# Optimization experiments

Measured on AMD Instinct MI355X. Metric: run time of the kernel, lower is better.

## Reference

```python
import jax, jax.numpy as jnp
import numpy as np
import math

NUM_HEADS = 16
HIDDEN = 1024
HEAD_DIM = HIDDEN // NUM_HEADS
WIN = 512  # relative position window size
B, S = 2, 2048
LN_EPS = 1e-5


def setup_inputs() -> dict:
    key = jax.random.key(0)
    ks = jax.random.split(key, 8)
    sd = 1.0 / math.sqrt(HIDDEN)
    return {
        "x": jax.random.normal(ks[0], (B, S, HIDDEN), jnp.float32),
        "Wq": jax.random.normal(ks[1], (HIDDEN, HIDDEN), jnp.float32) * sd,
        "bq": jnp.zeros((HIDDEN,), jnp.float32),
        "Wk": jax.random.normal(ks[2], (HIDDEN, HIDDEN), jnp.float32) * sd,
        "bk": jnp.zeros((HIDDEN,), jnp.float32),
        "Wv": jax.random.normal(ks[3], (HIDDEN, HIDDEN), jnp.float32) * sd,
        "bv": jnp.zeros((HIDDEN,), jnp.float32),
        "Wo": jax.random.normal(ks[4], (HIDDEN, HIDDEN), jnp.float32) * sd,
        "bo": jnp.zeros((HIDDEN,), jnp.float32),
        "relpos_table": jax.random.normal(ks[5], (WIN, HIDDEN), jnp.float32),
        "ln_gamma": jnp.ones((HIDDEN,), jnp.float32),
        "ln_beta": jnp.zeros((HIDDEN,), jnp.float32),
        "Wrk": jax.random.normal(ks[6], (HIDDEN, HIDDEN), jnp.float32) * sd,
        "brk": jnp.zeros((HIDDEN,), jnp.float32),
        "Wrq": jax.random.normal(ks[7], (HIDDEN, HIDDEN), jnp.float32) * sd,
        "brq": jnp.zeros((HIDDEN,), jnp.float32),
    }


def reference(x, Wq, bq, Wk, bk, Wv, bv, Wo, bo,
              relpos_table, ln_gamma, ln_beta, Wrk, brk, Wrq, brq):
    Bsz, Slen, H = x.shape
    nh, hd = NUM_HEADS, HEAD_DIM

    # QKV projections -> [B, S, nh, hd]
    q = (x @ Wq + bq).reshape(Bsz, Slen, nh, hd)
    k = (x @ Wk + bk).reshape(Bsz, Slen, nh, hd)
    v = (x @ Wv + bv).reshape(Bsz, Slen, nh, hd)

    mu = relpos_table.mean(-1, keepdims=True)
    var = relpos_table.var(-1, keepdims=True)  # biased, as in torch LayerNorm
    e = (relpos_table - mu) * jax.lax.rsqrt(var + LN_EPS) * ln_gamma + ln_beta

    # relative position index matrix [S, S]: clamp(key - query, -W+1, 0) + W-1
    qi = jnp.arange(Slen)
    relpos = jnp.clip(qi[None, :] - qi[:, None], -WIN + 1, 0) + (WIN - 1)

    rk = (e @ Wrk + brk).reshape(WIN, nh, hd)
    rq = (e @ Wrq + brq).reshape(WIN, nh, hd)

    # content-to-content scores [B, nh, S, S]
    c2c = jnp.einsum('bqhd,bkhd->bhqk', q, k)

    # content-to-position: scores over window then gather along window axis
    qps = jnp.einsum('bnhd,whd->bhnw', q, rk)           # [B, nh, S, W]
    c2p = qps[:, :, qi[:, None], relpos]                # [B, nh, S, S]

    # position-to-content: window x key_seq scores, gather along window axis
    kps = jnp.einsum('bnhd,whd->bhwn', k, rq)           # [B, nh, W, S]
    p2c = kps[:, :, relpos, qi[None, :]]                # [B, nh, S, S]

    scale_factor = 3.0  # 1 + relpos_q_enabled + relpos_k_enabled
    logits = (c2c + c2p + p2c) / math.sqrt(hd * scale_factor)

    # causal mask
    causal = qi[None, :] <= qi[:, None]
    logits = jnp.where(causal[None, None], logits, jnp.finfo(logits.dtype).min)

    attn = jax.nn.softmax(logits, axis=-1)              # [B, nh, S, S]
    out = jnp.einsum('bhqk,bkhd->bqhd', attn, v).reshape(Bsz, Slen, H)
    return out @ Wo + bo
```

## Files before the change

kernel.cpp:

```cpp
#include <hip/hip_runtime.h>
#include <math.h>

#define NH 16
#define HD 64
#define HID 1024
#define SEQ 2048
#define NB 2

typedef __attribute__((ext_vector_type(8))) short short8;
typedef __attribute__((ext_vector_type(4))) float f32x4;
typedef unsigned short u16;
typedef unsigned int u32;

constexpr float LN_EPS_C = 1e-5f;
constexpr float SM_SCALE = 0.07216878364870323f;

__device__ inline u16 f2b(float f) {
  unsigned u = __builtin_bit_cast(unsigned, f);
  u = (u + 0x7FFFu + ((u >> 16) & 1u)) >> 16;
  return (u16)u;
}
__device__ inline float b2f(u16 h) {
  unsigned u = ((unsigned)h) << 16;
  return __builtin_bit_cast(float, u);
}
__device__ inline u32 pk2(float lo, float hi) {
  return (u32)f2b(lo) | ((u32)f2b(hi) << 16);
}
__device__ inline f32x4 mfma16(short8 a, short8 b, f32x4 c) {
  return __builtin_amdgcn_mfma_f32_16x16x32_bf16(a, b, c, 0, 0, 0);
}
__device__ inline short8 swz8(const u16* base, int row, int hc) {
  return *reinterpret_cast<const short8*>(&base[row * 64 + 8 * (hc ^ (row & 7))]);
}
__device__ inline int vrot(int row, int col) {
  return row * 72 + ((col + 16 * ((row >> 3) & 3)) & 63);
}
template <int N>
__device__ inline float rorf(float x) {
  return __builtin_bit_cast(float,
      __builtin_amdgcn_update_dpp(0, __builtin_bit_cast(int, x),
                                  0x120 + N, 0xF, 0xF, true));
}
__device__ inline float rmax16(float x) {
  x = fmaxf(x, rorf<1>(x)); x = fmaxf(x, rorf<2>(x));
  x = fmaxf(x, rorf<4>(x)); x = fmaxf(x, rorf<8>(x));
  return x;
}
__device__ inline float rsum16(float x) {
  x += rorf<1>(x); x += rorf<2>(x); x += rorf<4>(x); x += rorf<8>(x);
  return x;
}

__global__ __launch_bounds__(256) void ln_kernel(const float* __restrict__ tbl,
    const float* __restrict__ gamma, const float* __restrict__ beta,
    u16* __restrict__ e) {
  int row = blockIdx.x;
  int t = threadIdx.x;
  const float4* rp = reinterpret_cast<const float4*>(tbl + (size_t)row * HID);
  float4 x = rp[t];
  float s = x.x + x.y + x.z + x.w;
  float ss = x.x * x.x + x.y * x.y + x.z * x.z + x.w * x.w;
  #pragma unroll
  for (int o = 1; o < 64; o <<= 1) {
    s += __shfl_xor(s, o);
    ss += __shfl_xor(ss, o);
  }
  __shared__ float sb[4], ssb[4];
  int w = t >> 6;
  if ((t & 63) == 0) { sb[w] = s; ssb[w] = ss; }
  __syncthreads();
  s = sb[0] + sb[1] + sb[2] + sb[3];
  ss = ssb[0] + ssb[1] + ssb[2] + ssb[3];
  float mu = s * (1.0f / HID);
  float var = ss * (1.0f / HID) - mu * mu;
  float rs = rsqrtf(var + LN_EPS_C);
  float4 g = reinterpret_cast<const float4*>(gamma)[t];
  float4 bt = reinterpret_cast<const float4*>(beta)[t];
  ushort4 o4;
  o4.x = f2b((x.x - mu) * rs * g.x + bt.x);
  o4.y = f2b((x.y - mu) * rs * g.y + bt.y);
  o4.z = f2b((x.z - mu) * rs * g.z + bt.z);
  o4.w = f2b((x.w - mu) * rs * g.w + bt.w);
  *reinterpret_cast<ushort4*>(&e[(size_t)row * HID + t * 4]) = o4;
}

__global__ __launch_bounds__(256) void conv_bf16(const float* __restrict__ src,
    u16* __restrict__ dst, int n) {
  int i = (blockIdx.x * 256 + threadIdx.x) * 8;
  if (i >= n) return;
  float4 a = *reinterpret_cast<const float4*>(&src[i]);
  float4 c = *reinterpret_cast<const float4*>(&src[i + 4]);
  short8 o;
  o[0] = (short)f2b(a.x); o[1] = (short)f2b(a.y); o[2] = (short)f2b(a.z); o[3] = (short)f2b(a.w);
  o[4] = (short)f2b(c.x); o[5] = (short)f2b(c.y); o[6] = (short)f2b(c.z); o[7] = (short)f2b(c.w);
  *reinterpret_cast<short8*>(&dst[i]) = o;
}

struct P6 {
  const float* s[6];
  u16* d[6];
};
__global__ __launch_bounds__(256) void transp_all(P6 p) {
  __shared__ float T[32][33];
  const float* W = p.s[blockIdx.z];
  u16* Wt = p.d[blockIdx.z];
  int bn = blockIdx.x * 32, bk = blockIdx.y * 32;
  int t = threadIdx.x;
  int r = t >> 3, c4 = (t & 7) * 4;
  float4 v = *reinterpret_cast<const float4*>(&W[(size_t)(bk + r) * HID + bn + c4]);
  T[r][c4 + 0] = v.x; T[r][c4 + 1] = v.y; T[r][c4 + 2] = v.z; T[r][c4 + 3] = v.w;
  __syncthreads();
  int n = t >> 3, k4 = (t & 7) * 4;
  ushort4 o;
  o.x = f2b(T[k4 + 0][n]); o.y = f2b(T[k4 + 1][n]);
  o.z = f2b(T[k4 + 2][n]); o.w = f2b(T[k4 + 3][n]);
  *reinterpret_cast<ushort4*>(&Wt[(size_t)(bn + n) * HID + bk + k4]) = o;
}

struct GO {
  const float* bias[3];
  void* out[3];
};
template <bool F32OUT>
__global__ __launch_bounds__(512) void gemm_bf16(const u16* __restrict__ A,
    const u16* __restrict__ Bt, GO go) {
  __shared__ u16 Al[8192];
  __shared__ u16 Bl[8192];
  int t = threadIdx.x;
  int gx = gridDim.x;
  int nwg = gx * gridDim.y;
  int lin = blockIdx.y * gx + blockIdx.x;
  lin = (lin & 7) * (nwg >> 3) + (lin >> 3);
  int cb = (lin % gx) * 128, rb = (lin / gx) * 128;
  int which = cb >> 10, cbl = cb & 1023;
  const float* bias = go.bias[which];
  void* Cout = go.out[which];
  int wv = t >> 6, lane = t & 63, l15 = lane & 15, lg = lane >> 4;
  int wr = (wv >> 2) * 64, wc = (wv & 3) * 32;
  int srow = t >> 2, sch = t & 3;
  f32x4 acc[4][2];
  #pragma unroll
  for (int i = 0; i < 4; ++i)
    #pragma unroll
    for (int j = 0; j < 2; ++j) acc[i][j] = (f32x4){0.f, 0.f, 0.f, 0.f};
  const u16* Ap = A + (size_t)(rb + srow) * HID;
  const u16* Bp = Bt + (size_t)(cb + srow) * HID;
  int slot0 = 8 * (sch ^ (srow & 7));
  int slot1 = 8 * ((sch + 4) ^ (srow & 7));
  short8 pa0 = *reinterpret_cast<const short8*>(&Ap[sch * 8]);
  short8 pa1 = *reinterpret_cast<const short8*>(&Ap[(sch + 4) * 8]);
  short8 pb0 = *reinterpret_cast<const short8*>(&Bp[sch * 8]);
  short8 pb1 = *reinterpret_cast<const short8*>(&Bp[(sch + 4) * 8]);
  for (int kk = 0; kk < HID; kk += 64) {
    __syncthreads();
    *reinterpret_cast<short8*>(&Al[srow * 64 + slot0]) = pa0;
    *reinterpret_cast<short8*>(&Al[srow * 64 + slot1]) = pa1;
    *reinterpret_cast<short8*>(&Bl[srow * 64 + slot0]) = pb0;
    *reinterpret_cast<short8*>(&Bl[srow * 64 + slot1]) = pb1;
    __syncthreads();
    if (kk + 64 < HID) {
      pa0 = *reinterpret_cast<const short8*>(&Ap[kk + 64 + sch * 8]);
      pa1 = *reinterpret_cast<const short8*>(&Ap[kk + 64 + (sch + 4) * 8]);
      pb0 = *reinterpret_cast<const short8*>(&Bp[kk + 64 + sch * 8]);
      pb1 = *reinterpret_cast<const short8*>(&Bp[kk + 64 + (sch + 4) * 8]);
    }
    #pragma unroll
    for (int s = 0; s < 2; ++s) {
      short8 am[4], bn[2];
      #pragma unroll
      for (int i = 0; i < 4; ++i) am[i] = swz8(Al, wr + i * 16 + l15, s * 4 + lg);
      #pragma unroll
      for (int j = 0; j < 2; ++j) bn[j] = swz8(Bl, wc + j * 16 + l15, s * 4 + lg);
      #pragma unroll
      for (int i = 0; i < 4; ++i)
        #pragma unroll
        for (int j = 0; j < 2; ++j)
          acc[i][j] = mfma16(am[i], bn[j], acc[i][j]);
    }
  }
  #pragma unroll
  for (int j = 0; j < 2; ++j) {
    float bv = bias[cbl + wc + j * 16 + l15];
    #pragma unroll
    for (int i = 0; i < 4; ++i) {
      #pragma unroll
      for (int r = 0; r < 4; ++r) {
        size_t idx = (size_t)(rb + wr + i * 16 + lg * 4 + r) * HID + cbl + wc + j * 16 + l15;
        float v = acc[i][j][r] + bv;
        if (F32OUT) reinterpret_cast<float*>(Cout)[idx] = v;
        else reinterpret_cast<u16*>(Cout)[idx] = f2b(v);
      }
    }
  }
}

template <bool F32OUT>
__global__ __launch_bounds__(256) void gemm_m64(const u16* __restrict__ A,
    const u16* __restrict__ Bt, GO go) {
  __shared__ u16 Al[4096];
  __shared__ u16 Bl[8192];
  int t = threadIdx.x;
  int gx = gridDim.x;
  int nwg = gx * gridDim.y;
  int lin = blockIdx.y * gx + blockIdx.x;
  lin = (lin & 7) * (nwg >> 3) + (lin >> 3);
  int cb = (lin % gx) * 128, rb = (lin / gx) * 64;
  int which = cb >> 10, cbl = cb & 1023;
  const float* bias = go.bias[which];
  void* Cout = go.out[which];
  int wv = t >> 6, lane = t & 63, l15 = lane & 15, lg = lane >> 4;
  int wc = wv * 32;
  int arow = t >> 2, ach = t & 3;
  int aslot0 = 8 * (ach ^ (arow & 7));
  int aslot1 = 8 * ((ach + 4) ^ (arow & 7));
  int brow = t >> 1, bch = (t & 1) * 4;
  const u16* Ap = A + (size_t)(rb + arow) * HID;
  const u16* Bp = Bt + (size_t)(cb + brow) * HID;
  f32x4 acc[4][2];
  #pragma unroll
  for (int i = 0; i < 4; ++i)
    #pragma unroll
    for (int j = 0; j < 2; ++j) acc[i][j] = (f32x4){0.f, 0.f, 0.f, 0.f};
  short8 pa0 = *reinterpret_cast<const short8*>(&Ap[ach * 8]);
  short8 pa1 = *reinterpret_cast<const short8*>(&Ap[(ach + 4) * 8]);
  short8 pb[4];
  #pragma unroll
  for (int j = 0; j < 4; ++j)
    pb[j] = *reinterpret_cast<const short8*>(&Bp[(bch + j) * 8]);
  for (int kk = 0; kk < HID; kk += 64) {
    __syncthreads();
    *reinterpret_cast<short8*>(&Al[arow * 64 + aslot0]) = pa0;
    *reinterpret_cast<short8*>(&Al[arow * 64 + aslot1]) = pa1;
    #pragma unroll
    for (int j = 0; j < 4; ++j)
      *reinterpret_cast<short8*>(&Bl[brow * 64 + 8 * ((bch + j) ^ (brow & 7))]) = pb[j];
    __syncthreads();
    if (kk + 64 < HID) {
      pa0 = *reinterpret_cast<const short8*>(&Ap[kk + 64 + ach * 8]);
      pa1 = *reinterpret_cast<const short8*>(&Ap[kk + 64 + (ach + 4) * 8]);
      #pragma unroll
      for (int j = 0; j < 4; ++j)
        pb[j] = *reinterpret_cast<const short8*>(&Bp[kk + 64 + (bch + j) * 8]);
    }
    #pragma unroll
    for (int s = 0; s < 2; ++s) {
      short8 am[4], bn[2];
      #pragma unroll
      for (int i = 0; i < 4; ++i) am[i] = swz8(Al, i * 16 + l15, s * 4 + lg);
      #pragma unroll
      for (int j = 0; j < 2; ++j) bn[j] = swz8(Bl, wc + j * 16 + l15, s * 4 + lg);
      #pragma unroll
      for (int i = 0; i < 4; ++i)
        #pragma unroll
        for (int j = 0; j < 2; ++j)
          acc[i][j] = mfma16(am[i], bn[j], acc[i][j]);
    }
  }
  #pragma unroll
  for (int j = 0; j < 2; ++j) {
    float bv = bias[cbl + wc + j * 16 + l15];
    #pragma unroll
    for (int i = 0; i < 4; ++i) {
      #pragma unroll
      for (int r = 0; r < 4; ++r) {
        size_t idx = (size_t)(rb + i * 16 + lg * 4 + r) * HID + cbl + wc + j * 16 + l15;
        float v = acc[i][j][r] + bv;
        if (F32OUT) reinterpret_cast<float*>(Cout)[idx] = v;
        else reinterpret_cast<u16*>(Cout)[idx] = f2b(v);
      }
    }
  }
}

__global__ __launch_bounds__(256) void biasqk(const u16* __restrict__ Qb,
    const u16* __restrict__ Kb, const u16* __restrict__ RKb,
    const u16* __restrict__ RQb, float* __restrict__ qrk0,
    float* __restrict__ krq0) {
  int o = blockIdx.x * 64 + (threadIdx.x >> 2);
  int sub = threadIdx.x & 3;
  int b = o >> 15, h = (o >> 11) & 15, i = o & 2047;
  size_t rbase = (size_t)(b * SEQ + i) * HID + h * HD + sub * 16;
  size_t tbase = (size_t)h * HD + sub * 16;
  float s1 = 0.f, s2 = 0.f;
  #pragma unroll
  for (int c = 0; c < 2; ++c) {
    short8 qv = *reinterpret_cast<const short8*>(&Qb[rbase + c * 8]);
    short8 rv = *reinterpret_cast<const short8*>(&RKb[tbase + c * 8]);
    short8 kv = *reinterpret_cast<const short8*>(&Kb[rbase + c * 8]);
    short8 uv = *reinterpret_cast<const short8*>(&RQb[tbase + c * 8]);
    #pragma unroll
    for (int j = 0; j < 8; ++j) {
      s1 += b2f((u16)qv[j]) * b2f((u16)rv[j]);
      s2 += b2f((u16)kv[j]) * b2f((u16)uv[j]);
    }
  }
  s1 += __shfl_xor(s1, 1); s1 += __shfl_xor(s1, 2);
  s2 += __shfl_xor(s2, 1); s2 += __shfl_xor(s2, 2);
  if (sub == 0) { qrk0[o] = s1 * SM_SCALE; krq0[o] = s2 * SM_SCALE; }
}

__global__ __launch_bounds__(256, 3) void bias_kernel(
    const u16* __restrict__ Qb, const u16* __restrict__ Kb,
    const u16* __restrict__ RKb, const u16* __restrict__ RQb,
    u16* __restrict__ bandT) {
  __shared__ u16 smem[20992];
  const int KsO = 0, UO = 4096;
  const int RKO = UO, RQO = UO + 8192;
  const int G1O = UO, G2O = UO + 8448;

  int qt = blockIdx.x;
  int h = blockIdx.y, b = blockIdx.z;
  int q0 = qt * 64;
  int t = threadIdx.x;
  int wv = t >> 6, lane = t & 63, l15 = lane & 15, lg = lane >> 4;
  int qs = q0 + wv * 16;
  int hoff = h * HD;

  size_t qgrow = (size_t)(b * SEQ + qs + l15) * HID + hoff;
  short8 aq0 = *reinterpret_cast<const short8*>(&Qb[qgrow + lg * 8]);
  short8 aq1 = *reinterpret_cast<const short8*>(&Qb[qgrow + 32 + lg * 8]);

  const f32x4 Z = (f32x4){0.f, 0.f, 0.f, 0.f};
  int vr = t >> 2, vc8 = (t & 3) * 8;
  int ktlo = qt - 8; if (ktlo < 0) ktlo = 0;
  size_t tbase = (((size_t)(b * NH + h) * 32 + qt) * 9) << 12;

  for (int kt = ktlo; kt <= qt; ++kt) {
    int k0 = kt * 64;
    int dt = qt - kt;
    int wlo = 448 - 64 * dt; if (wlo < 0) wlo = 0;
    __syncthreads();
    {
      const u16* kg = &Kb[(size_t)(b * SEQ + k0 + vr) * HID + hoff];
      int c0 = vc8 >> 3;
      *reinterpret_cast<short8*>(&smem[KsO + vr * 64 + 8 * (c0 ^ (vr & 7))]) =
          *reinterpret_cast<const short8*>(&kg[vc8]);
      *reinterpret_cast<short8*>(&smem[KsO + vr * 64 + 8 * ((c0 + 4) ^ (vr & 7))]) =
          *reinterpret_cast<const short8*>(&kg[vc8 + 32]);
    }
    for (int e2 = t; e2 < 1024; e2 += 256) {
      int rr = e2 >> 3, cch = e2 & 7;
      int wr2 = wlo + rr; if (wr2 > 511) wr2 = 511;
      size_t gb = (size_t)wr2 * HID + hoff + cch * 8;
      int slot = 8 * (cch ^ (rr & 7));
      *reinterpret_cast<short8*>(&smem[RKO + rr * 64 + slot]) =
          *reinterpret_cast<const short8*>(&RKb[gb]);
      *reinterpret_cast<short8*>(&smem[RQO + rr * 64 + slot]) =
          *reinterpret_cast<const short8*>(&RQb[gb]);
    }
    __syncthreads();
    u32 g1p[16], g2p[16];
    #pragma unroll
    for (int cw = 0; cw < 8; ++cw) {
      short8 r0 = swz8(&smem[RKO], cw * 16 + l15, lg);
      short8 r1 = swz8(&smem[RKO], cw * 16 + l15, 4 + lg);
      f32x4 g = mfma16(r1, aq1, mfma16(r0, aq0, Z));
      g1p[2 * cw] = pk2(g[0], g[1]);
      g1p[2 * cw + 1] = pk2(g[2], g[3]);
    }
    short8 kw0 = swz8(&smem[KsO], wv * 16 + l15, lg);
    short8 kw1 = swz8(&smem[KsO], wv * 16 + l15, 4 + lg);
    #pragma unroll
    for (int cw = 0; cw < 8; ++cw) {
      short8 u0 = swz8(&smem[RQO], cw * 16 + l15, lg);
      short8 u1 = swz8(&smem[RQO], cw * 16 + l15, 4 + lg);
      f32x4 g = mfma16(u1, kw1, mfma16(u0, kw0, Z));
      g2p[2 * cw] = pk2(g[0], g[1]);
      g2p[2 * cw + 1] = pk2(g[2], g[3]);
    }
    __syncthreads();
    #pragma unroll
    for (int cw = 0; cw < 8; ++cw) {
      *reinterpret_cast<uint2*>(&smem[G1O + (wv * 16 + l15) * 132 + cw * 16 + lg * 4]) =
          make_uint2(g1p[2 * cw], g1p[2 * cw + 1]);
      *reinterpret_cast<uint2*>(&smem[G2O + (wv * 16 + l15) * 132 + cw * 16 + lg * 4]) =
          make_uint2(g2p[2 * cw], g2p[2 * cw + 1]);
    }
    __syncthreads();
    u16* outp = bandT + tbase + ((size_t)dt << 12) + t * 16;
    #pragma unroll
    for (int c = 0; c < 4; ++c) {
      float vv[4];
      #pragma unroll
      for (int r = 0; r < 4; ++r) {
        int q = qs + lg * 4 + r;
        int k = k0 + c * 16 + l15;
        int wi = 511 - (q - k) - wlo; if (wi < 0) wi = 0;
        vv[r] = (b2f(smem[G1O + (wv * 16 + lg * 4 + r) * 132 + wi]) +
                 b2f(smem[G2O + (c * 16 + l15) * 132 + wi])) * SM_SCALE;
      }
      *reinterpret_cast<uint2*>(outp + c * 4) =
          make_uint2(pk2(vv[0], vv[1]), pk2(vv[2], vv[3]));
    }
  }
}

__global__ __launch_bounds__(256, 2) void attn_mfma(
    const u16* __restrict__ Qb, const u16* __restrict__ Kb,
    const u16* __restrict__ Vb, const float* __restrict__ qrk0,
    const float* __restrict__ krq0, const u16* __restrict__ bandT,
    u16* __restrict__ ATT) {
  __shared__ u16 smem[22016];
  const int KsB[2] = {0, 4096};
  const int VtB[2] = {8192, 12800};
  const int PsO = 17408;

  int qtA = 31 - (int)blockIdx.x;
  int qtB = (int)blockIdx.x;
  int h = blockIdx.y, b = blockIdx.z;
  int t = threadIdx.x;
  int wv = t >> 6, lane = t & 63, l15 = lane & 15, lg = lane >> 4;
  int hoff = h * HD;
  int bh = (b * NH + h) * SEQ;
  size_t tbaseA = (((size_t)(b * NH + h) * 32 + qtA) * 9) << 12;
  size_t tbaseB = (((size_t)(b * NH + h) * 32 + qtB) * 9) << 12;

  int qsA = qtA * 64 + wv * 16;
  int qsB = qtB * 64 + wv * 16;
  size_t qgA = (size_t)(b * SEQ + qsA + l15) * HID + hoff;
  size_t qgB = (size_t)(b * SEQ + qsB + l15) * HID + hoff;
  short8 aqA0 = *reinterpret_cast<const short8*>(&Qb[qgA + lg * 8]);
  short8 aqA1 = *reinterpret_cast<const short8*>(&Qb[qgA + 32 + lg * 8]);
  short8 aqB0 = *reinterpret_cast<const short8*>(&Qb[qgB + lg * 8]);
  short8 aqB1 = *reinterpret_cast<const short8*>(&Qb[qgB + 32 + lg * 8]);
  float qb0A[4], qb0B[4];
  #pragma unroll
  for (int r = 0; r < 4; ++r) {
    qb0A[r] = qrk0[bh + qsA + lg * 4 + r];
    qb0B[r] = qrk0[bh + qsB + lg * 4 + r];
  }

  float mA[4], lA[4], mB[4], lB[4];
  f32x4 oA[4], oB[4];
  #pragma unroll
  for (int r = 0; r < 4; ++r) { mA[r] = -INFINITY; lA[r] = 0.f; mB[r] = -INFINITY; lB[r] = 0.f; }
  #pragma unroll
  for (int c = 0; c < 4; ++c) {
    oA[c] = (f32x4){0.f, 0.f, 0.f, 0.f};
    oB[c] = (f32x4){0.f, 0.f, 0.f, 0.f};
  }

  const f32x4 Z = (f32x4){0.f, 0.f, 0.f, 0.f};
  int vr = t >> 2, vc8 = (t & 3) * 8;
  int c0s = vc8 >> 3;
  int kslot0 = vr * 64 + 8 * (c0s ^ (vr & 7));
  int kslot1 = vr * 64 + 8 * ((c0s + 4) ^ (vr & 7));
  int vslot[16];
  #pragma unroll
  for (int j = 0; j < 8; ++j) {
    vslot[j] = vrot(vc8 + j, vr);
    vslot[8 + j] = vrot(vc8 + 32 + j, vr);
  }

  {
    const u16* kg = &Kb[(size_t)(b * SEQ + vr) * HID + hoff];
    short8 k0v = *reinterpret_cast<const short8*>(&kg[vc8]);
    short8 k1v = *reinterpret_cast<const short8*>(&kg[vc8 + 32]);
    *reinterpret_cast<short8*>(&smem[KsB[0] + kslot0]) = k0v;
    *reinterpret_cast<short8*>(&smem[KsB[0] + kslot1]) = k1v;
    const u16* vg = &Vb[(size_t)(b * SEQ + vr) * HID + hoff];
    short8 v0v = *reinterpret_cast<const short8*>(&vg[vc8]);
    short8 v1v = *reinterpret_cast<const short8*>(&vg[vc8 + 32]);
    #pragma unroll
    for (int j = 0; j < 8; ++j) smem[VtB[0] + vslot[j]] = (u16)v0v[j];
    #pragma unroll
    for (int j = 0; j < 8; ++j) smem[VtB[0] + vslot[8 + j]] = (u16)v1v[j];
  }
  __syncthreads();

  int cur = 0;
  for (int kt = 0; kt <= qtA; ++kt) {
    int k0 = kt * 64;
    int dtA = qtA - kt;
    bool doB = (kt <= qtB);
    int dtB = qtB - kt;
    bool bandedA = (dtA <= 8);
    bool bandedB = doB && (dtB <= 8);
    int ksb = KsB[cur], vtb = VtB[cur];
    int ksn = KsB[cur ^ 1], vtn = VtB[cur ^ 1];

    short8 pA0, pA1, pB0, pB1;
    if (bandedA) {
      const u16* tb = bandT + tbaseA + ((size_t)dtA << 12) + t * 16;
      pA0 = *reinterpret_cast<const short8*>(tb);
      pA1 = *reinterpret_cast<const short8*>(tb + 8);
    }
    if (bandedB) {
      const u16* tb = bandT + tbaseB + ((size_t)dtB << 12) + t * 16;
      pB0 = *reinterpret_cast<const short8*>(tb);
      pB1 = *reinterpret_cast<const short8*>(tb + 8);
    }
    float kq[4];
    if (dtA > 8 || (doB && dtB > 8)) {
      #pragma unroll
      for (int c = 0; c < 4; ++c) kq[c] = krq0[bh + k0 + c * 16 + l15];
    }
    short8 nk0, nk1, nv0, nv1;
    if (kt < qtA) {
      const u16* kg = &Kb[(size_t)(b * SEQ + k0 + 64 + vr) * HID + hoff];
      nk0 = *reinterpret_cast<const short8*>(&kg[vc8]);
      nk1 = *reinterpret_cast<const short8*>(&kg[vc8 + 32]);
      const u16* vg = &Vb[(size_t)(b * SEQ + k0 + 64 + vr) * HID + hoff];
      nv0 = *reinterpret_cast<const short8*>(&vg[vc8]);
      nv1 = *reinterpret_cast<const short8*>(&vg[vc8 + 32]);
    }

    short8 kb0[4], kb1[4];
    #pragma unroll
    for (int c = 0; c < 4; ++c) {
      kb0[c] = swz8(&smem[ksb], c * 16 + l15, lg);
      kb1[c] = swz8(&smem[ksb], c * 16 + l15, 4 + lg);
    }
    f32x4 sA[4], sB[4];
    #pragma unroll
    for (int c = 0; c < 4; ++c)
      sA[c] = mfma16(aqA1, kb1[c], mfma16(aqA0, kb0[c], Z));
    if (doB) {
      #pragma unroll
      for (int c = 0; c < 4; ++c)
        sB[c] = mfma16(aqB1, kb1[c], mfma16(aqB0, kb0[c], Z));
    }
    #pragma unroll
    for (int c = 0; c < 4; ++c) {
      #pragma unroll
      for (int r = 0; r < 4; ++r) {
        float bbv = bandedA ? b2f((u16)((c < 2 ? pA0 : pA1)[(c & 1) * 4 + r]))
                            : qb0A[r] + kq[c];
        float v = fmaf(sA[c][r], SM_SCALE, bbv);
        if (dtA == 0) {
          int ql = wv * 16 + lg * 4 + r, kl = c * 16 + l15;
          if (ql < kl) v = -INFINITY;
        }
        sA[c][r] = v;
      }
    }
    if (doB) {
      #pragma unroll
      for (int c = 0; c < 4; ++c) {
        #pragma unroll
        for (int r = 0; r < 4; ++r) {
          float bbv = bandedB ? b2f((u16)((c < 2 ? pB0 : pB1)[(c & 1) * 4 + r]))
                              : qb0B[r] + kq[c];
          float v = fmaf(sB[c][r], SM_SCALE, bbv);
          if (dtB == 0) {
            int ql = wv * 16 + lg * 4 + r, kl = c * 16 + l15;
            if (ql < kl) v = -INFINITY;
          }
          sB[c][r] = v;
        }
      }
    }
    float alA[4], alB[4];
    #pragma unroll
    for (int r = 0; r < 4; ++r) {
      float mx = fmaxf(fmaxf(sA[0][r], sA[1][r]), fmaxf(sA[2][r], sA[3][r]));
      mx = rmax16(mx);
      float mn = fmaxf(mA[r], mx);
      alA[r] = __expf(mA[r] - mn);
      float ps = 0.f;
      #pragma unroll
      for (int c = 0; c < 4; ++c) {
        float p = __expf(sA[c][r] - mn);
        sA[c][r] = p;
        ps += p;
      }
      ps = rsum16(ps);
      lA[r] = lA[r] * alA[r] + ps;
      mA[r] = mn;
    }
    if (doB) {
      #pragma unroll
      for (int r = 0; r < 4; ++r) {
        float mx = fmaxf(fmaxf(sB[0][r], sB[1][r]), fmaxf(sB[2][r], sB[3][r]));
        mx = rmax16(mx);
        float mn = fmaxf(mB[r], mx);
        alB[r] = __expf(mB[r] - mn);
        float ps = 0.f;
        #pragma unroll
        for (int c = 0; c < 4; ++c) {
          float p = __expf(sB[c][r] - mn);
          sB[c][r] = p;
          ps += p;
        }
        ps = rsum16(ps);
        lB[r] = lB[r] * alB[r] + ps;
        mB[r] = mn;
      }
    }
    short8 vb0[4], vb1[4];
    #pragma unroll
    for (int c = 0; c < 4; ++c) {
      int n = c * 16 + l15;
      vb0[c] = *reinterpret_cast<const short8*>(&smem[vtb + vrot(n, lg * 8)]);
      vb1[c] = *reinterpret_cast<const short8*>(&smem[vtb + vrot(n, 32 + lg * 8)]);
    }
    #pragma unroll
    for (int c = 0; c < 4; ++c) {
      #pragma unroll
      for (int r = 0; r < 4; ++r) {
        smem[PsO + vrot(wv * 16 + lg * 4 + r, c * 16 + l15)] = f2b(sA[c][r]);
        oA[c][r] *= alA[r];
      }
    }
    int prow = wv * 16 + l15;
    {
      short8 ap0 = *reinterpret_cast<const short8*>(&smem[PsO + vrot(prow, lg * 8)]);
      short8 ap1 = *reinterpret_cast<const short8*>(&smem[PsO + vrot(prow, 32 + lg * 8)]);
      #pragma unroll
      for (int c = 0; c < 4; ++c)
        oA[c] = mfma16(ap1, vb1[c], mfma16(ap0, vb0[c], oA[c]));
    }
    if (doB) {
      #pragma unroll
      for (int c = 0; c < 4; ++c) {
        #pragma unroll
        for (int r = 0; r < 4; ++r) {
          smem[PsO + vrot(wv * 16 + lg * 4 + r, c * 16 + l15)] = f2b(sB[c][r]);
          oB[c][r] *= alB[r];
        }
      }
      short8 bp0 = *reinterpret_cast<const short8*>(&smem[PsO + vrot(prow, lg * 8)]);
      short8 bp1 = *reinterpret_cast<const short8*>(&smem[PsO + vrot(prow, 32 + lg * 8)]);
      #pragma unroll
      for (int c = 0; c < 4; ++c)
        oB[c] = mfma16(bp1, vb1[c], mfma16(bp0, vb0[c], oB[c]));
    }
    if (kt < qtA) {
      *reinterpret_cast<short8*>(&smem[ksn + kslot0]) = nk0;
      *reinterpret_cast<short8*>(&smem[ksn + kslot1]) = nk1;
      #pragma unroll
      for (int j = 0; j < 8; ++j) smem[vtn + vslot[j]] = (u16)nv0[j];
      #pragma unroll
      for (int j = 0; j < 8; ++j) smem[vtn + vslot[8 + j]] = (u16)nv1[j];
    }
    __syncthreads();
    cur ^= 1;
  }
  #pragma unroll
  for (int r = 0; r < 4; ++r) { lA[r] = 1.0f / lA[r]; lB[r] = 1.0f / lB[r]; }
  #pragma unroll
  for (int c = 0; c < 4; ++c) {
    #pragma unroll
    for (int r = 0; r < 4; ++r) {
      size_t obA = (size_t)(b * SEQ + qsA + lg * 4 + r) * HID + hoff + c * 16 + l15;
      ATT[obA] = f2b(oA[c][r] * lA[r]);
      size_t obB = (size_t)(b * SEQ + qsB + lg * 4 + r) * HID + hoff + c * 16 + l15;
      ATT[obB] = f2b(oB[c][r] * lB[r]);
    }
  }
}

extern "C" void kernel_launch(void* const* d_in, const int* in_sizes, int n_in,
                              void* d_out, int out_size, void* d_ws, size_t ws_size,
                              hipStream_t stream) {
  const float* x      = (const float*)d_in[0];
  const float* Wq     = (const float*)d_in[1];
  const float* bq     = (const float*)d_in[2];
  const float* Wk     = (const float*)d_in[3];
  const float* bk     = (const float*)d_in[4];
  const float* Wv     = (const float*)d_in[5];
  const float* bv     = (const float*)d_in[6];
  const float* Wo     = (const float*)d_in[7];
  const float* bo     = (const float*)d_in[8];
  const float* relpos = (const float*)d_in[9];
  const float* gamma  = (const float*)d_in[10];
  const float* beta   = (const float*)d_in[11];
  const float* Wrk    = (const float*)d_in[12];
  const float* brk    = (const float*)d_in[13];
  const float* Wrq    = (const float*)d_in[14];
  const float* brq    = (const float*)d_in[15];
  float* out = (float*)d_out;

  u16* wsu = (u16*)d_ws;
  size_t off = 0;
  auto alloc = [&](size_t n) { u16* p = wsu + off; off += n; return p; };
  u16* xb   = alloc(4194304);
  u16* Eb   = alloc(524288);
  u16* WtQ  = alloc(1048576);
  u16* WtK  = alloc(1048576);
  u16* WtV  = alloc(1048576);
  u16* WtO  = alloc(1048576);
  u16* WtRK = alloc(1048576);
  u16* WtRQ = alloc(1048576);
  u16* Qb2  = alloc(4194304);
  u16* Kb2  = alloc(4194304);
  u16* Vb2  = alloc(4194304);
  u16* ATTb = alloc(4194304);
  u16* RKb2 = alloc(524288);
  u16* RQb2 = alloc(524288);
  float* qrk0 = (float*)(wsu + off); off += 131072;
  float* krq0 = (float*)(wsu + off); off += 131072;
  u16* bandT = alloc((size_t)NB * NH * 32 * 9 * 4096);

  ln_kernel<<<512, 256, 0, stream>>>(relpos, gamma, beta, Eb);
  conv_bf16<<<2048, 256, 0, stream>>>(x, xb, 4194304);
  P6 p6;
  p6.s[0] = Wq; p6.s[1] = Wk; p6.s[2] = Wv; p6.s[3] = Wo; p6.s[4] = Wrk; p6.s[5] = Wrq;
  p6.d[0] = WtQ; p6.d[1] = WtK; p6.d[2] = WtV; p6.d[3] = WtO; p6.d[4] = WtRK; p6.d[5] = WtRQ;
  dim3 gT(32, 32, 6);
  transp_all<<<gT, 256, 0, stream>>>(p6);

  GO goQKV = {{bq, bk, bv}, {Qb2, Kb2, Vb2}};
  dim3 gQKV(24, 32);
  gemm_bf16<false><<<gQKV, 512, 0, stream>>>(xb, WtQ, goQKV);
  GO goRel = {{brk, brq, brq}, {RKb2, RQb2, RQb2}};
  dim3 gRel2(16, 8);
  gemm_m64<false><<<gRel2, 256, 0, stream>>>(Eb, WtRK, goRel);

  biasqk<<<1024, 256, 0, stream>>>(Qb2, Kb2, RKb2, RQb2, qrk0, krq0);

  dim3 gB(32, NH, NB);
  bias_kernel<<<gB, 256, 0, stream>>>(Qb2, Kb2, RKb2, RQb2, bandT);

  dim3 gA(16, NH, NB);
  attn_mfma<<<gA, 256, 0, stream>>>(Qb2, Kb2, Vb2, qrk0, krq0, bandT, ATTb);

  GO goOut = {{bo, bo, bo}, {out, out, out}};
  dim3 gOut(8, 64);
  gemm_m64<true><<<gOut, 256, 0, stream>>>(ATTb, WtO, goOut);
}
```

Before: 219.9 us.

## Merge prep kernels, fold biasqk into bias kernel, skip unchanged softmax rescale

Combines the layernorm, input conversion and weight transpose launches into one prep kernel that dispatches on block index. Computes the per-row qrk0/krq0 bias scalars inside bias_kernel instead of a separate launch. In the attention loop, the online-softmax rescale of the accumulators is skipped when no row max changes across the wavefront. Together these remove three launches and some multiplies, at the cost of a branch and a wave vote per tile.

```diff
diff --git a/kernel.cpp b/kernel.cpp
--- a/kernel.cpp
+++ b/kernel.cpp
@@ -52,70 +52,67 @@
   return x;
 }
 
-__global__ __launch_bounds__(256) void ln_kernel(const float* __restrict__ tbl,
-    const float* __restrict__ gamma, const float* __restrict__ beta,
-    u16* __restrict__ e) {
-  int row = blockIdx.x;
+struct PrepArgs {
+  const float* tbl; const float* gamma; const float* beta; u16* e;
+  const float* x; u16* xb;
+  const float* ws[6]; u16* wd[6];
+};
+__global__ __launch_bounds__(256) void prep_kernel(PrepArgs p) {
+  __shared__ float T[32][33];
+  __shared__ float sb[4], ssb[4];
+  int bid = blockIdx.x;
   int t = threadIdx.x;
-  const float4* rp = reinterpret_cast<const float4*>(tbl + (size_t)row * HID);
-  float4 x = rp[t];
-  float s = x.x + x.y + x.z + x.w;
-  float ss = x.x * x.x + x.y * x.y + x.z * x.z + x.w * x.w;
-  #pragma unroll
-  for (int o = 1; o < 64; o <<= 1) {
-    s += __shfl_xor(s, o);
-    ss += __shfl_xor(ss, o);
-  }
-  __shared__ float sb[4], ssb[4];
-  int w = t >> 6;
-  if ((t & 63) == 0) { sb[w] = s; ssb[w] = ss; }
-  __syncthreads();
-  s = sb[0] + sb[1] + sb[2] + sb[3];
-  ss = ssb[0] + ssb[1] + ssb[2] + ssb[3];
-  float mu = s * (1.0f / HID);
-  float var = ss * (1.0f / HID) - mu * mu;
-  float rs = rsqrtf(var + LN_EPS_C);
-  float4 g = reinterpret_cast<const float4*>(gamma)[t];
-  float4 bt = reinterpret_cast<const float4*>(beta)[t];
-  ushort4 o4;
-  o4.x = f2b((x.x - mu) * rs * g.x + bt.x);
-  o4.y = f2b((x.y - mu) * rs * g.y + bt.y);
-  o4.z = f2b((x.z - mu) * rs * g.z + bt.z);
-  o4.w = f2b((x.w - mu) * rs * g.w + bt.w);
-  *reinterpret_cast<ushort4*>(&e[(size_t)row * HID + t * 4]) = o4;
-}
-
-__global__ __launch_bounds__(256) void conv_bf16(const float* __restrict__ src,
-    u16* __restrict__ dst, int n) {
-  int i = (blockIdx.x * 256 + threadIdx.x) * 8;
-  if (i >= n) return;
-  float4 a = *reinterpret_cast<const float4*>(&src[i]);
-  float4 c = *reinterpret_cast<const float4*>(&src[i + 4]);
-  short8 o;
-  o[0] = (short)f2b(a.x); o[1] = (short)f2b(a.y); o[2] = (short)f2b(a.z); o[3] = (short)f2b(a.w);
-  o[4] = (short)f2b(c.x); o[5] = (short)f2b(c.y); o[6] = (short)f2b(c.z); o[7] = (short)f2b(c.w);
-  *reinterpret_cast<short8*>(&dst[i]) = o;
-}
-
-struct P6 {
-  const float* s[6];
-  u16* d[6];
-};
-__global__ __launch_bounds__(256) void transp_all(P6 p) {
-  __shared__ float T[32][33];
-  const float* W = p.s[blockIdx.z];
-  u16* Wt = p.d[blockIdx.z];
-  int bn = blockIdx.x * 32, bk = blockIdx.y * 32;
-  int t = threadIdx.x;
-  int r = t >> 3, c4 = (t & 7) * 4;
-  float4 v = *reinterpret_cast<const float4*>(&W[(size_t)(bk + r) * HID + bn + c4]);
-  T[r][c4 + 0] = v.x; T[r][c4 + 1] = v.y; T[r][c4 + 2] = v.z; T[r][c4 + 3] = v.w;
-  __syncthreads();
-  int n = t >> 3, k4 = (t & 7) * 4;
-  ushort4 o;
-  o.x = f2b(T[k4 + 0][n]); o.y = f2b(T[k4 + 1][n]);
-  o.z = f2b(T[k4 + 2][n]); o.w = f2b(T[k4 + 3][n]);
-  *reinterpret_cast<ushort4*>(&Wt[(size_t)(bn + n) * HID + bk + k4]) = o;
+  if (bid < 512) {
+    int row = bid;
+    const float4* rp = reinterpret_cast<const float4*>(p.tbl + (size_t)row * HID);
+    float4 x = rp[t];
+    float s = x.x + x.y + x.z + x.w;
+    float ss = x.x * x.x + x.y * x.y + x.z * x.z + x.w * x.w;
+    #pragma unroll
+    for (int o = 1; o < 64; o <<= 1) {
+      s += __shfl_xor(s, o);
+      ss += __shfl_xor(ss, o);
+    }
+    int w = t >> 6;
+    if ((t & 63) == 0) { sb[w] = s; ssb[w] = ss; }
+    __syncthreads();
+    s = sb[0] + sb[1] + sb[2] + sb[3];
+    ss = ssb[0] + ssb[1] + ssb[2] + ssb[3];
+    float mu = s * (1.0f / HID);
+    float var = ss * (1.0f / HID) - mu * mu;
+    float rs = rsqrtf(var + LN_EPS_C);
+    float4 g = reinterpret_cast<const float4*>(p.gamma)[t];
+    float4 bt = reinterpret_cast<const float4*>(p.beta)[t];
+    ushort4 o4;
+    o4.x = f2b((x.x - mu) * rs * g.x + bt.x);
+    o4.y = f2b((x.y - mu) * rs * g.y + bt.y);
+    o4.z = f2b((x.z - mu) * rs * g.z + bt.z);
+    o4.w = f2b((x.w - mu) * rs * g.w + bt.w);
+    *reinterpret_cast<ushort4*>(&p.e[(size_t)row * HID + t * 4]) = o4;
+  } else if (bid < 2560) {
+    int i = ((bid - 512) * 256 + t) * 8;
+    float4 a = *reinterpret_cast<const float4*>(&p.x[i]);
+    float4 c = *reinterpret_cast<const float4*>(&p.x[i + 4]);
+    short8 o;
+    o[0] = (short)f2b(a.x); o[1] = (short)f2b(a.y); o[2] = (short)f2b(a.z); o[3] = (short)f2b(a.w);
+    o[4] = (short)f2b(c.x); o[5] = (short)f2b(c.y); o[6] = (short)f2b(c.z); o[7] = (short)f2b(c.w);
+    *reinterpret_cast<short8*>(&p.xb[i]) = o;
+  } else {
+    int z = (bid - 2560) >> 10;
+    int rem = (bid - 2560) & 1023;
+    int bn = (rem & 31) * 32, bk = (rem >> 5) * 32;
+    const float* W = p.ws[z];
+    u16* Wt = p.wd[z];
+    int r = t >> 3, c4 = (t & 7) * 4;
+    float4 v = *reinterpret_cast<const float4*>(&W[(size_t)(bk + r) * HID + bn + c4]);
+    T[r][c4 + 0] = v.x; T[r][c4 + 1] = v.y; T[r][c4 + 2] = v.z; T[r][c4 + 3] = v.w;
+    __syncthreads();
+    int n = t >> 3, k4 = (t & 7) * 4;
+    ushort4 o;
+    o.x = f2b(T[k4 + 0][n]); o.y = f2b(T[k4 + 1][n]);
+    o.z = f2b(T[k4 + 2][n]); o.w = f2b(T[k4 + 3][n]);
+    *reinterpret_cast<ushort4*>(&Wt[(size_t)(bn + n) * HID + bk + k4]) = o;
+  }
 }
 
 struct GO {
@@ -273,37 +270,11 @@
   }
 }
 
-__global__ __launch_bounds__(256) void biasqk(const u16* __restrict__ Qb,
-    const u16* __restrict__ Kb, const u16* __restrict__ RKb,
-    const u16* __restrict__ RQb, float* __restrict__ qrk0,
-    float* __restrict__ krq0) {
-  int o = blockIdx.x * 64 + (threadIdx.x >> 2);
-  int sub = threadIdx.x & 3;
-  int b = o >> 15, h = (o >> 11) & 15, i = o & 2047;
-  size_t rbase = (size_t)(b * SEQ + i) * HID + h * HD + sub * 16;
-  size_t tbase = (size_t)h * HD + sub * 16;
-  float s1 = 0.f, s2 = 0.f;
-  #pragma unroll
-  for (int c = 0; c < 2; ++c) {
-    short8 qv = *reinterpret_cast<const short8*>(&Qb[rbase + c * 8]);
-    short8 rv = *reinterpret_cast<const short8*>(&RKb[tbase + c * 8]);
-    short8 kv = *reinterpret_cast<const short8*>(&Kb[rbase + c * 8]);
-    short8 uv = *reinterpret_cast<const short8*>(&RQb[tbase + c * 8]);
-    #pragma unroll
-    for (int j = 0; j < 8; ++j) {
-      s1 += b2f((u16)qv[j]) * b2f((u16)rv[j]);
-      s2 += b2f((u16)kv[j]) * b2f((u16)uv[j]);
-    }
-  }
-  s1 += __shfl_xor(s1, 1); s1 += __shfl_xor(s1, 2);
-  s2 += __shfl_xor(s2, 1); s2 += __shfl_xor(s2, 2);
-  if (sub == 0) { qrk0[o] = s1 * SM_SCALE; krq0[o] = s2 * SM_SCALE; }
-}
-
 __global__ __launch_bounds__(256, 3) void bias_kernel(
     const u16* __restrict__ Qb, const u16* __restrict__ Kb,
     const u16* __restrict__ RKb, const u16* __restrict__ RQb,
-    u16* __restrict__ bandT) {
+    u16* __restrict__ bandT, float* __restrict__ qrk0,
+    float* __restrict__ krq0) {
   __shared__ u16 smem[20992];
   const int KsO = 0, UO = 4096;
   const int RKO = UO, RQO = UO + 8192;
@@ -316,6 +287,30 @@
   int wv = t >> 6, lane = t & 63, l15 = lane & 15, lg = lane >> 4;
   int qs = q0 + wv * 16;
   int hoff = h * HD;
+  int bh = (b * NH + h) * SEQ;
+
+  {
+    int i = q0 + (t >> 2);
+    int sub = t & 3;
+    size_t rbase = (size_t)(b * SEQ + i) * HID + hoff + sub * 16;
+    size_t tb2 = (size_t)hoff + sub * 16;
+    float s1 = 0.f, s2 = 0.f;
+    #pragma unroll
+    for (int c = 0; c < 2; ++c) {
+      short8 qv = *reinterpret_cast<const short8*>(&Qb[rbase + c * 8]);
+      short8 rv = *reinterpret_cast<const short8*>(&RKb[tb2 + c * 8]);
+      short8 kv = *reinterpret_cast<const short8*>(&Kb[rbase + c * 8]);
+      short8 uv = *reinterpret_cast<const short8*>(&RQb[tb2 + c * 8]);
+      #pragma unroll
+      for (int j = 0; j < 8; ++j) {
+        s1 += b2f((u16)qv[j]) * b2f((u16)rv[j]);
+        s2 += b2f((u16)kv[j]) * b2f((u16)uv[j]);
+      }
+    }
+    s1 += __shfl_xor(s1, 1); s1 += __shfl_xor(s1, 2);
+    s2 += __shfl_xor(s2, 1); s2 += __shfl_xor(s2, 2);
+    if (sub == 0) { qrk0[bh + i] = s1 * SM_SCALE; krq0[bh + i] = s2 * SM_SCALE; }
+  }
 
   size_t qgrow = (size_t)(b * SEQ + qs + l15) * HID + hoff;
   short8 aq0 = *reinterpret_cast<const short8*>(&Qb[qgrow + lg * 8]);
@@ -551,41 +546,70 @@
         }
       }
     }
-    float alA[4], alB[4];
-    #pragma unroll
-    for (int r = 0; r < 4; ++r) {
-      float mx = fmaxf(fmaxf(sA[0][r], sA[1][r]), fmaxf(sA[2][r], sA[3][r]));
-      mx = rmax16(mx);
-      float mn = fmaxf(mA[r], mx);
-      alA[r] = __expf(mA[r] - mn);
-      float ps = 0.f;
-      #pragma unroll
-      for (int c = 0; c < 4; ++c) {
-        float p = __expf(sA[c][r] - mn);
-        sA[c][r] = p;
-        ps += p;
-      }
-      ps = rsum16(ps);
-      lA[r] = lA[r] * alA[r] + ps;
-      mA[r] = mn;
+    {
+      float mn[4];
+      #pragma unroll
+      for (int r = 0; r < 4; ++r) {
+        float mx = fmaxf(fmaxf(sA[0][r], sA[1][r]), fmaxf(sA[2][r], sA[3][r]));
+        mx = rmax16(mx);
+        mn[r] = fmaxf(mA[r], mx);
+      }
+      bool sk = (mn[0] == mA[0]) && (mn[1] == mA[1]) &&
+                (mn[2] == mA[2]) && (mn[3] == mA[3]);
+      if (!__all(sk)) {
+        #pragma unroll
+        for (int r = 0; r < 4; ++r) {
+          float al = __expf(mA[r] - mn[r]);
+          lA[r] *= al;
+          mA[r] = mn[r];
+          #pragma unroll
+          for (int c = 0; c < 4; ++c) oA[c][r] *= al;
+        }
+      }
+      #pragma unroll
+      for (int r = 0; r < 4; ++r) {
+        float ps = 0.f;
+        #pragma unroll
+        for (int c = 0; c < 4; ++c) {
+          float p = __expf(sA[c][r] - mA[r]);
+          sA[c][r] = p;
+          ps += p;
+        }
+        ps = rsum16(ps);
+        lA[r] += ps;
+      }
     }
     if (doB) {
+      float mn[4];
       #pragma unroll
       for (int r = 0; r < 4; ++r) {
         float mx = fmaxf(fmaxf(sB[0][r], sB[1][r]), fmaxf(sB[2][r], sB[3][r]));
         mx = rmax16(mx);
-        float mn = fmaxf(mB[r], mx);
-        alB[r] = __expf(mB[r] - mn);
+        mn[r] = fmaxf(mB[r], mx);
+      }
+      bool sk = (mn[0] == mB[0]) && (mn[1] == mB[1]) &&
+                (mn[2] == mB[2]) && (mn[3] == mB[3]);
+      if (!__all(sk)) {
+        #pragma unroll
+        for (int r = 0; r < 4; ++r) {
+          float al = __expf(mB[r] - mn[r]);
+          lB[r] *= al;
+          mB[r] = mn[r];
+          #pragma unroll
+          for (int c = 0; c < 4; ++c) oB[c][r] *= al;
+        }
+      }
+      #pragma unroll
+      for (int r = 0; r < 4; ++r) {
         float ps = 0.f;
         #pragma unroll
         for (int c = 0; c < 4; ++c) {
-          float p = __expf(sB[c][r] - mn);
+          float p = __expf(sB[c][r] - mB[r]);
           sB[c][r] = p;
           ps += p;
         }
         ps = rsum16(ps);
-        lB[r] = lB[r] * alB[r] + ps;
-        mB[r] = mn;
+        lB[r] += ps;
       }
     }
     short8 vb0[4], vb1[4];
@@ -596,13 +620,10 @@
       vb1[c] = *reinterpret_cast<const short8*>(&smem[vtb + vrot(n, 32 + lg * 8)]);
     }
     #pragma unroll
-    for (int c = 0; c < 4; ++c) {
-      #pragma unroll
-      for (int r = 0; r < 4; ++r) {
+    for (int c = 0; c < 4; ++c)
+      #pragma unroll
+      for (int r = 0; r < 4; ++r)
         smem[PsO + vrot(wv * 16 + lg * 4 + r, c * 16 + l15)] = f2b(sA[c][r]);
-        oA[c][r] *= alA[r];
-      }
-    }
     int prow = wv * 16 + l15;
     {
       short8 ap0 = *reinterpret_cast<const short8*>(&smem[PsO + vrot(prow, lg * 8)]);
@@ -613,13 +634,10 @@
     }
     if (doB) {
       #pragma unroll
-      for (int c = 0; c < 4; ++c) {
+      for (int c = 0; c < 4; ++c)
         #pragma unroll
-        for (int r = 0; r < 4; ++r) {
+        for (int r = 0; r < 4; ++r)
           smem[PsO + vrot(wv * 16 + lg * 4 + r, c * 16 + l15)] = f2b(sB[c][r]);
-          oB[c][r] *= alB[r];
-        }
-      }
       short8 bp0 = *reinterpret_cast<const short8*>(&smem[PsO + vrot(prow, lg * 8)]);
       short8 bp1 = *reinterpret_cast<const short8*>(&smem[PsO + vrot(prow, 32 + lg * 8)]);
       #pragma unroll
@@ -693,13 +711,12 @@
   float* krq0 = (float*)(wsu + off); off += 131072;
   u16* bandT = alloc((size_t)NB * NH * 32 * 9 * 4096);
 
-  ln_kernel<<<512, 256, 0, stream>>>(relpos, gamma, beta, Eb);
-  conv_bf16<<<2048, 256, 0, stream>>>(x, xb, 4194304);
-  P6 p6;
-  p6.s[0] = Wq; p6.s[1] = Wk; p6.s[2] = Wv; p6.s[3] = Wo; p6.s[4] = Wrk; p6.s[5] = Wrq;
-  p6.d[0] = WtQ; p6.d[1] = WtK; p6.d[2] = WtV; p6.d[3] = WtO; p6.d[4] = WtRK; p6.d[5] = WtRQ;
-  dim3 gT(32, 32, 6);
-  transp_all<<<gT, 256, 0, stream>>>(p6);
+  PrepArgs pa;
+  pa.tbl = relpos; pa.gamma = gamma; pa.beta = beta; pa.e = Eb;
+  pa.x = x; pa.xb = xb;
+  pa.ws[0] = Wq; pa.ws[1] = Wk; pa.ws[2] = Wv; pa.ws[3] = Wo; pa.ws[4] = Wrk; pa.ws[5] = Wrq;
+  pa.wd[0] = WtQ; pa.wd[1] = WtK; pa.wd[2] = WtV; pa.wd[3] = WtO; pa.wd[4] = WtRK; pa.wd[5] = WtRQ;
+  prep_kernel<<<8704, 256, 0, stream>>>(pa);
 
   GO goQKV = {{bq, bk, bv}, {Qb2, Kb2, Vb2}};
   dim3 gQKV(24, 32);
@@ -708,10 +725,8 @@
   dim3 gRel2(16, 8);
   gemm_m64<false><<<gRel2, 256, 0, stream>>>(Eb, WtRK, goRel);
 
-  biasqk<<<1024, 256, 0, stream>>>(Qb2, Kb2, RKb2, RQb2, qrk0, krq0);
-
   dim3 gB(32, NH, NB);
-  bias_kernel<<<gB, 256, 0, stream>>>(Qb2, Kb2, RKb2, RQb2, bandT);
+  bias_kernel<<<gB, 256, 0, stream>>>(Qb2, Kb2, RKb2, RQb2, bandT, qrk0, krq0);
 
   dim3 gA(16, NH, NB);
   attn_mfma<<<gA, 256, 0, stream>>>(Qb2, Kb2, Vb2, qrk0, krq0, bandT, ATTb);
```

Measured after the change: 215.3 us. -2.1%, faster.
